# Kernel tuning notes

Hardware: AMD Instinct MI355X
Metric: run time of the kernel (lower is better)

The kernel has to match this reference:

```python
import jax, jax.numpy as jnp
import numpy as np

U = 64  # LSTM_UNITS

def _lstm(xt, kernel, rec, bias):
    # xt: [B, T, 4U]; keras LSTM gate order i, f, g(c), o
    B = xt.shape[0]
    h0 = jnp.zeros((B, U), xt.dtype)
    c0 = jnp.zeros((B, U), xt.dtype)
    def step(carry, x):
        h, c = carry
        z = x @ kernel + h @ rec + bias  # [B, 4U]
        i, f, g, o = jnp.split(z, 4, axis=-1)
        i = jax.nn.sigmoid(i); f = jax.nn.sigmoid(f)
        g = jnp.tanh(g); o = jax.nn.sigmoid(o)
        c = f * c + i * g
        h = o * jnp.tanh(c)
        return (h, c), h
    _, hs = jax.lax.scan(step, (h0, c0), jnp.swapaxes(xt, 0, 1))
    return jnp.swapaxes(hs, 0, 1)  # [B, T, U]

def setup_inputs() -> dict:
    key = jax.random.key(0)
    ks = jax.random.split(key, 12)
    B, T, P = 8, 100, 1000
    pro_id = jax.random.randint(ks[0], (B, T), 0, P, dtype=jnp.int32)
    label = jax.random.randint(ks[1], (B, T), 0, 2, dtype=jnp.int32)
    X = jax.random.normal(ks[2], (P, 2 * U), jnp.float32)
    cos_X = jax.random.uniform(ks[3], (P, P), jnp.float32)
    trimatrix = jnp.tril(jnp.ones((T, T), jnp.float32))  # causal mask [s, t]
    onehot_table = jax.random.normal(ks[4], (2, 4 * U), jnp.float32)
    s = 0.05
    lstm_kernel = jax.random.normal(ks[5], (4 * U, 4 * U), jnp.float32) * s
    lstm_rec = jax.random.normal(ks[6], (U, 4 * U), jnp.float32) * s
    lstm_bias = jnp.zeros((4 * U,), jnp.float32)
    W1 = jax.random.normal(ks[7], (3 * U, 50), jnp.float32) * s
    b1 = jnp.zeros((50,), jnp.float32)
    W2 = jax.random.normal(ks[8], (50, 1), jnp.float32) * s
    b2 = jnp.zeros((1,), jnp.float32)
    return {"pro_id": pro_id, "label": label, "num_pro": P, "X": X,
            "cos_X": cos_X, "trimatrix": trimatrix, "onehot_table": onehot_table,
            "lstm_kernel": lstm_kernel, "lstm_rec": lstm_rec, "lstm_bias": lstm_bias,
            "W1": W1, "b1": b1, "W2": W2, "b2": b2}

def reference(pro_id, label, num_pro, X, cos_X, trimatrix, onehot_table,
              lstm_kernel, lstm_rec, lstm_bias, W1, b1, W2, b2):
    B, T = pro_id.shape
    # one_hot @ X  ==  gather rows of X
    t_X = jnp.tile(X[pro_id], (1, 1, 2))           # [B, T, 4U]
    label_emb = onehot_table[label]                 # [B, T, 4U]
    xt = t_X * label_emb
    ht = _lstm(xt, lstm_kernel, lstm_rec, lstm_bias)  # [B, T, U]
    a = cos_X[pro_id]                               # [B, T, P] (one_hot @ cos_X)
    # ajhj[b,t,p,u] = sum_s tri[s,t] * a[b,s,p] * ht[b,s,u]  (causal weighted sum)
    ajhj = jnp.einsum('bsp,bsu,st->btpu', a, ht, trimatrix)
    XX = jnp.broadcast_to(X[None, None], (B, T, num_pro, 2 * U))
    hatt = jnp.concatenate([ajhj, XX], axis=-1)     # [B, T, P, 3U]
    r = jax.nn.relu(hatt @ W1 + b1)                 # [B, T, P, 50]
    prediction = r @ W2 + b2                        # [B, T, P, 1]
    return prediction
```

## Files before the change

### kernel.cpp

```cpp
#include <hip/hip_runtime.h>
#include <math.h>

#define BB 8
#define TT 100
#define PP 1000
#define UU 64
#define NJ 52
#define GROW 56


__global__ __launch_bounds__(256) void k1_xk(const int* __restrict__ pro_id,
    const int* __restrict__ label, const float* __restrict__ X,
    const float* __restrict__ onehot, const float* __restrict__ kern,
    const float* __restrict__ bias, float* __restrict__ xk)
{
    __shared__ __align__(16) float xt[8][256];
    const int j = threadIdx.x;
    const int r0 = blockIdx.x * 8;
    for (int r = 0; r < 8; ++r) {
        int row = r0 + r;
        int pid = pro_id[row];
        int lab = label[row];
        xt[r][j] = X[pid * 128 + (j & 127)] * onehot[lab * 256 + j];
    }
    __syncthreads();
    float acc[8];
    float bj = bias[j];
#pragma unroll
    for (int r = 0; r < 8; ++r) acc[r] = bj;
    for (int k4 = 0; k4 < 256; k4 += 4) {
        float4 xv[8];
#pragma unroll
        for (int r = 0; r < 8; ++r) xv[r] = *(const float4*)&xt[r][k4];
#pragma unroll
        for (int kk = 0; kk < 4; ++kk) {
            float kv = kern[(k4 + kk) * 256 + j];
#pragma unroll
            for (int r = 0; r < 8; ++r) {
                float x = (kk == 0) ? xv[r].x : (kk == 1) ? xv[r].y : (kk == 2) ? xv[r].z : xv[r].w;
                acc[r] += x * kv;
            }
        }
    }
#pragma unroll
    for (int r = 0; r < 8; ++r) xk[(r0 + r) * 256 + j] = acc[r];
}

__global__ __launch_bounds__(256) void k2_lstm(const float* __restrict__ xk,
    const float* __restrict__ rec, float* __restrict__ ht)
{
    __shared__ __align__(16) float h_sh[64];
    __shared__ float zs[256];
    const int j = threadIdx.x;
    const int b = blockIdx.x;
    float reccol[64];
#pragma unroll
    for (int u = 0; u < 64; ++u) reccol[u] = rec[u * 256 + j];
    float c = 0.f;
    if (j < 64) h_sh[j] = 0.f;
    __syncthreads();
    for (int t = 0; t < TT; ++t) {
        float z = xk[(b * TT + t) * 256 + j];
#pragma unroll
        for (int u4 = 0; u4 < 16; ++u4) {
            float4 h4 = *(const float4*)&h_sh[u4 * 4];
            z += h4.x * reccol[u4 * 4 + 0] + h4.y * reccol[u4 * 4 + 1]
               + h4.z * reccol[u4 * 4 + 2] + h4.w * reccol[u4 * 4 + 3];
        }
        float act;
        if (j >= 128 && j < 192) {
            act = 2.f / (1.f + __expf(-2.f * z)) - 1.f;
        } else {
            act = 1.f / (1.f + __expf(-z));
        }
        zs[j] = act;
        __syncthreads();
        if (j < 64) {
            float gi = zs[j], gf = zs[j + 64], gg = zs[j + 128], go = zs[j + 192];
            c = gf * c + gi * gg;
            float th = 2.f / (1.f + __expf(-2.f * c)) - 1.f;
            float h = go * th;
            h_sh[j] = h;
            ht[(b * TT + t) * 64 + j] = h;
        }
        __syncthreads();
    }
}

__global__ __launch_bounds__(256) void k3_xct(const float* __restrict__ X,
    const float* __restrict__ W1, const float* __restrict__ b1,
    float* __restrict__ XcT)
{
    int n = blockIdx.x * 256 + threadIdx.x;
    if (n >= GROW * PP) return;
    int jrow = n / PP;
    int p = n - jrow * PP;
    float acc = 0.f;
    if (jrow < 50) {
        acc = b1[jrow];
        for (int k = 0; k < 128; ++k)
            acc += X[p * 128 + k] * W1[(64 + k) * 50 + jrow];
    }
    XcT[n] = acc;
}

__global__ __launch_bounds__(64) void kg(const float* __restrict__ ht,
    const float* __restrict__ W1, float* __restrict__ G)
{
    __shared__ float hsh[64];
    const int row = blockIdx.x;
    const int j = threadIdx.x;
    hsh[j] = ht[row * 64 + j];
    __syncthreads();
    float acc = 0.f;
    if (j < 50) {
#pragma unroll
        for (int u = 0; u < 64; ++u) acc += hsh[u] * W1[u * 50 + j];
    }
    if (j < GROW) G[row * GROW + j] = acc;
}

__global__ __launch_bounds__(256) void k4_main(const int* __restrict__ pro_id,
    const float* __restrict__ cos_X, const float* __restrict__ XcT,
    const float* __restrict__ G, const float* __restrict__ W2,
    const float* __restrict__ b2, float* __restrict__ out)
{
    const int b = blockIdx.z;
    const int p = blockIdx.y * 256 + threadIdx.x;
    const int ci = blockIdx.x;
    const int t0 = ci * 7;
    const int t1 = (t0 + 7 < TT) ? (t0 + 7) : TT;
    const bool valid = p < PP;
    const int pc = valid ? p : 0;

    float V[NJ];
#pragma unroll
    for (int jj = 0; jj < NJ; ++jj) V[jj] = XcT[jj * PP + pc];
    const float b2v = b2[0];

    for (int s = TT - 1; s >= t0; --s) {
        int pid = pro_id[b * TT + s];
        float a = cos_X[pid * PP + pc];
        const float4* G4 = (const float4*)(G + (b * TT + s) * GROW);
#pragma unroll
        for (int jv = 0; jv < 13; ++jv) {
            float4 g = G4[jv];
            V[4 * jv + 0] += a * g.x;
            V[4 * jv + 1] += a * g.y;
            V[4 * jv + 2] += a * g.z;
            V[4 * jv + 3] += a * g.w;
        }
        if (s < t1) {
            float acc = b2v;
#pragma unroll
            for (int jv = 0; jv < 12; ++jv) {
                float4 w = *(const float4*)&W2[4 * jv];
                acc += w.x * fmaxf(V[4 * jv + 0], 0.f)
                     + w.y * fmaxf(V[4 * jv + 1], 0.f)
                     + w.z * fmaxf(V[4 * jv + 2], 0.f)
                     + w.w * fmaxf(V[4 * jv + 3], 0.f);
            }
            acc += W2[48] * fmaxf(V[48], 0.f) + W2[49] * fmaxf(V[49], 0.f);
            if (valid) out[(b * TT + s) * PP + p] = acc;
        }
    }
}

extern "C" void kernel_launch(void* const* d_in, const int* in_sizes, int n_in,
                              void* d_out, int out_size, void* d_ws, size_t ws_size,
                              hipStream_t stream)
{
    const int* pro_id  = (const int*)d_in[0];
    const int* label   = (const int*)d_in[1];
    const float* X     = (const float*)d_in[3];
    const float* cos_X = (const float*)d_in[4];
    const float* onehot = (const float*)d_in[6];
    const float* lk    = (const float*)d_in[7];
    const float* lr    = (const float*)d_in[8];
    const float* lb    = (const float*)d_in[9];
    const float* W1    = (const float*)d_in[10];
    const float* b1    = (const float*)d_in[11];
    const float* W2    = (const float*)d_in[12];
    const float* b2    = (const float*)d_in[13];

    float* ws  = (float*)d_ws;
    float* xk  = ws;
    float* ht  = ws + 204800;
    float* XcT = ws + 256000;
    float* G   = ws + 312000;
    float* out = (float*)d_out;

    hipLaunchKernelGGL(k1_xk,  dim3(100),      dim3(256), 0, stream, pro_id, label, X, onehot, lk, lb, xk);
    hipLaunchKernelGGL(k3_xct, dim3(219),      dim3(256), 0, stream, X, W1, b1, XcT);
    hipLaunchKernelGGL(k2_lstm,dim3(8),        dim3(256), 0, stream, xk, lr, ht);
    hipLaunchKernelGGL(kg,     dim3(800),      dim3(64),  0, stream, ht, W1, G);
    hipLaunchKernelGGL(k4_main,dim3(15, 4, 8), dim3(256), 0, stream, pro_id, cos_X, XcT, G, W2, b2, out);
}
```

Before: 216.4 us.

## Fuse prep kernels, shuffle-based LSTM gate exchange, fold G projection into LSTM

Merges the xk projection and the X·W1 precompute into one launch by splitting on block index. The X·W1 part now stages X transposed in shared memory. The LSTM kernel lays threads out so each wavefront holds all four gates for 16 units, so gates are exchanged with shuffles and one barrier per step is removed. It also prefetches the next xk value, splits the dot product into four accumulators, and keeps every h in shared memory so the G = h·W1 projection runs at the end of the same kernel. This cuts launch count and the serial per-step latency, but the G projection now runs on only 8 blocks.

Result: slower. 273.6 us (+26.4%).

```diff
diff --git a/kernel.cpp b/kernel.cpp
--- a/kernel.cpp
+++ b/kernel.cpp
@@ -4,120 +4,170 @@
 #define BB 8
 #define TT 100
 #define PP 1000
-#define UU 64
 #define NJ 52
 #define GROW 56
-
-
-__global__ __launch_bounds__(256) void k1_xk(const int* __restrict__ pro_id,
+#define HSTRIDE 68
+
+
+__global__ __launch_bounds__(256) void prep(const int* __restrict__ pro_id,
     const int* __restrict__ label, const float* __restrict__ X,
     const float* __restrict__ onehot, const float* __restrict__ kern,
-    const float* __restrict__ bias, float* __restrict__ xk)
-{
-    __shared__ __align__(16) float xt[8][256];
-    const int j = threadIdx.x;
-    const int r0 = blockIdx.x * 8;
-    for (int r = 0; r < 8; ++r) {
-        int row = r0 + r;
-        int pid = pro_id[row];
-        int lab = label[row];
-        xt[r][j] = X[pid * 128 + (j & 127)] * onehot[lab * 256 + j];
-    }
+    const float* __restrict__ bias, const float* __restrict__ W1,
+    const float* __restrict__ b1, float* __restrict__ xk, float* __restrict__ XcT)
+{
+    __shared__ __align__(16) float smem[128 * 65];
+    const int tid = threadIdx.x;
+
+    if (blockIdx.x < 100) {
+        float (*xt)[256] = (float(*)[256])smem;
+        const int j = tid;
+        const int r0 = blockIdx.x * 8;
+        for (int r = 0; r < 8; ++r) {
+            int row = r0 + r;
+            int pid = pro_id[row];
+            int lab = label[row];
+            xt[r][j] = X[pid * 128 + (j & 127)] * onehot[lab * 256 + j];
+        }
+        __syncthreads();
+        float acc[8];
+        float bj = bias[j];
+#pragma unroll
+        for (int r = 0; r < 8; ++r) acc[r] = bj;
+        for (int k4 = 0; k4 < 256; k4 += 4) {
+            float4 xv[8];
+#pragma unroll
+            for (int r = 0; r < 8; ++r) xv[r] = *(const float4*)&xt[r][k4];
+#pragma unroll
+            for (int kk = 0; kk < 4; ++kk) {
+                float kv = kern[(k4 + kk) * 256 + j];
+#pragma unroll
+                for (int r = 0; r < 8; ++r) {
+                    float x = (kk == 0) ? xv[r].x : (kk == 1) ? xv[r].y : (kk == 2) ? xv[r].z : xv[r].w;
+                    acc[r] += x * kv;
+                }
+            }
+        }
+#pragma unroll
+        for (int r = 0; r < 8; ++r) xk[(r0 + r) * 256 + j] = acc[r];
+    } else {
+        const int p0 = (blockIdx.x - 100) * 64;
+#pragma unroll
+        for (int r = 0; r < 8; ++r) {
+            int flat = (tid + 256 * r) * 4;
+            int i = flat >> 7;
+            int k = flat & 127;
+            int p = p0 + i;
+            float4 v = make_float4(0.f, 0.f, 0.f, 0.f);
+            if (p < PP) v = *(const float4*)&X[p * 128 + k];
+            smem[(k + 0) * 65 + i] = v.x;
+            smem[(k + 1) * 65 + i] = v.y;
+            smem[(k + 2) * 65 + i] = v.z;
+            smem[(k + 3) * 65 + i] = v.w;
+        }
+        __syncthreads();
+        const int ploc = tid & 63;
+        const int j0 = tid >> 6;
+        float acc[13];
+#pragma unroll
+        for (int m = 0; m < 13; ++m) {
+            int j = j0 + 4 * m;
+            acc[m] = (j < 50) ? b1[j] : 0.f;
+        }
+        for (int k = 0; k < 128; ++k) {
+            float xv = smem[k * 65 + ploc];
+            const float* w1r = &W1[(64 + k) * 50];
+#pragma unroll
+            for (int m = 0; m < 13; ++m) {
+                int j = j0 + 4 * m;
+                if (j < 50) acc[m] += xv * w1r[j];
+            }
+        }
+        int p = p0 + ploc;
+        if (p < PP) {
+#pragma unroll
+            for (int m = 0; m < 13; ++m) {
+                int j = j0 + 4 * m;
+                if (j < 50) XcT[j * PP + p] = acc[m];
+            }
+        }
+        for (int idx = tid; idx < 6 * 64; idx += 256) {
+            int r = 50 + (idx >> 6);
+            int pp = p0 + (idx & 63);
+            if (pp < PP) XcT[r * PP + pp] = 0.f;
+        }
+    }
+}
+
+__global__ __launch_bounds__(256) void k2_lstm(const float* __restrict__ xk,
+    const float* __restrict__ rec, const float* __restrict__ W1,
+    float* __restrict__ G)
+{
+    __shared__ __align__(16) float h_all[(TT + 1) * HSTRIDE];
+    const int tid = threadIdx.x;
+    const int b = blockIdx.x;
+    const int l = tid & 63;
+    const int w = tid >> 6;
+    const int u = (w << 4) | (l & 15);
+    const int g = l >> 4;
+    const int col = (g << 6) | u;
+
+    float rcol[64];
+#pragma unroll
+    for (int u2 = 0; u2 < 64; ++u2) rcol[u2] = rec[u2 * 256 + col];
+
+    if (tid < 64) h_all[tid] = 0.f;
+    float c = 0.f;
+    const float* xkb = xk + b * TT * 256;
+    float zc = xkb[col];
     __syncthreads();
-    float acc[8];
-    float bj = bias[j];
-#pragma unroll
-    for (int r = 0; r < 8; ++r) acc[r] = bj;
-    for (int k4 = 0; k4 < 256; k4 += 4) {
-        float4 xv[8];
-#pragma unroll
-        for (int r = 0; r < 8; ++r) xv[r] = *(const float4*)&xt[r][k4];
-#pragma unroll
-        for (int kk = 0; kk < 4; ++kk) {
-            float kv = kern[(k4 + kk) * 256 + j];
-#pragma unroll
-            for (int r = 0; r < 8; ++r) {
-                float x = (kk == 0) ? xv[r].x : (kk == 1) ? xv[r].y : (kk == 2) ? xv[r].z : xv[r].w;
-                acc[r] += x * kv;
-            }
-        }
-    }
-#pragma unroll
-    for (int r = 0; r < 8; ++r) xk[(r0 + r) * 256 + j] = acc[r];
-}
-
-__global__ __launch_bounds__(256) void k2_lstm(const float* __restrict__ xk,
-    const float* __restrict__ rec, float* __restrict__ ht)
-{
-    __shared__ __align__(16) float h_sh[64];
-    __shared__ float zs[256];
-    const int j = threadIdx.x;
-    const int b = blockIdx.x;
-    float reccol[64];
-#pragma unroll
-    for (int u = 0; u < 64; ++u) reccol[u] = rec[u * 256 + j];
-    float c = 0.f;
-    if (j < 64) h_sh[j] = 0.f;
-    __syncthreads();
+
     for (int t = 0; t < TT; ++t) {
-        float z = xk[(b * TT + t) * 256 + j];
-#pragma unroll
-        for (int u4 = 0; u4 < 16; ++u4) {
-            float4 h4 = *(const float4*)&h_sh[u4 * 4];
-            z += h4.x * reccol[u4 * 4 + 0] + h4.y * reccol[u4 * 4 + 1]
-               + h4.z * reccol[u4 * 4 + 2] + h4.w * reccol[u4 * 4 + 3];
-        }
+        float a0 = zc, a1 = 0.f, a2 = 0.f, a3 = 0.f;
+        if (t < TT - 1) zc = xkb[(t + 1) * 256 + col];
+        const float4* h4p = (const float4*)&h_all[t * HSTRIDE];
+#pragma unroll
+        for (int m = 0; m < 16; ++m) {
+            float4 hv = h4p[m];
+            a0 += hv.x * rcol[4 * m + 0];
+            a1 += hv.y * rcol[4 * m + 1];
+            a2 += hv.z * rcol[4 * m + 2];
+            a3 += hv.w * rcol[4 * m + 3];
+        }
+        float z = (a0 + a1) + (a2 + a3);
         float act;
-        if (j >= 128 && j < 192) {
-            act = 2.f / (1.f + __expf(-2.f * z)) - 1.f;
-        } else {
-            act = 1.f / (1.f + __expf(-z));
-        }
-        zs[j] = act;
+        if (g == 2) act = 2.f / (1.f + __expf(-2.f * z)) - 1.f;
+        else        act = 1.f / (1.f + __expf(-z));
+        const int base = l & 15;
+        float gi = __shfl(act, base);
+        float gf = __shfl(act, base + 16);
+        float gg = __shfl(act, base + 32);
+        float go = __shfl(act, base + 48);
+        c = gf * c + gi * gg;
+        float h = go * (2.f / (1.f + __expf(-2.f * c)) - 1.f);
+        if (g == 0) h_all[(t + 1) * HSTRIDE + u] = h;
         __syncthreads();
-        if (j < 64) {
-            float gi = zs[j], gf = zs[j + 64], gg = zs[j + 128], go = zs[j + 192];
-            c = gf * c + gi * gg;
-            float th = 2.f / (1.f + __expf(-2.f * c)) - 1.f;
-            float h = go * th;
-            h_sh[j] = h;
-            ht[(b * TT + t) * 64 + j] = h;
-        }
-        __syncthreads();
-    }
-}
-
-__global__ __launch_bounds__(256) void k3_xct(const float* __restrict__ X,
-    const float* __restrict__ W1, const float* __restrict__ b1,
-    float* __restrict__ XcT)
-{
-    int n = blockIdx.x * 256 + threadIdx.x;
-    if (n >= GROW * PP) return;
-    int jrow = n / PP;
-    int p = n - jrow * PP;
-    float acc = 0.f;
-    if (jrow < 50) {
-        acc = b1[jrow];
-        for (int k = 0; k < 128; ++k)
-            acc += X[p * 128 + k] * W1[(64 + k) * 50 + jrow];
-    }
-    XcT[n] = acc;
-}
-
-__global__ __launch_bounds__(64) void kg(const float* __restrict__ ht,
-    const float* __restrict__ W1, float* __restrict__ G)
-{
-    __shared__ float hsh[64];
-    const int row = blockIdx.x;
-    const int j = threadIdx.x;
-    hsh[j] = ht[row * 64 + j];
-    __syncthreads();
-    float acc = 0.f;
-    if (j < 50) {
-#pragma unroll
-        for (int u = 0; u < 64; ++u) acc += hsh[u] * W1[u * 50 + j];
-    }
-    if (j < GROW) G[row * GROW + j] = acc;
+    }
+
+    const int brow0 = b * TT;
+    for (int idx = tid; idx < TT * 13; idx += 256) {
+        int row = idx / 13;
+        int m = idx - row * 13;
+        int j = 4 * m;
+        const float* hrow = &h_all[(row + 1) * HSTRIDE];
+        float ax = 0.f, ay = 0.f, az = 0.f, aw = 0.f;
+#pragma unroll 16
+        for (int u2 = 0; u2 < 64; ++u2) {
+            float hv = hrow[u2];
+            const float* wp = &W1[u2 * 50 + j];
+            ax += hv * wp[0];
+            ay += hv * wp[1];
+            az += hv * wp[2];
+            aw += hv * wp[3];
+        }
+        if (m == 12) { az = 0.f; aw = 0.f; }
+        float4 o = make_float4(ax, ay, az, aw);
+        *(float4*)&G[(brow0 + row) * GROW + j] = o;
+    }
 }
 
 __global__ __launch_bounds__(256) void k4_main(const int* __restrict__ pro_id,
@@ -144,21 +194,21 @@
         const float4* G4 = (const float4*)(G + (b * TT + s) * GROW);
 #pragma unroll
         for (int jv = 0; jv < 13; ++jv) {
-            float4 g = G4[jv];
-            V[4 * jv + 0] += a * g.x;
-            V[4 * jv + 1] += a * g.y;
-            V[4 * jv + 2] += a * g.z;
-            V[4 * jv + 3] += a * g.w;
+            float4 gv = G4[jv];
+            V[4 * jv + 0] += a * gv.x;
+            V[4 * jv + 1] += a * gv.y;
+            V[4 * jv + 2] += a * gv.z;
+            V[4 * jv + 3] += a * gv.w;
         }
         if (s < t1) {
             float acc = b2v;
 #pragma unroll
             for (int jv = 0; jv < 12; ++jv) {
-                float4 w = *(const float4*)&W2[4 * jv];
-                acc += w.x * fmaxf(V[4 * jv + 0], 0.f)
-                     + w.y * fmaxf(V[4 * jv + 1], 0.f)
-                     + w.z * fmaxf(V[4 * jv + 2], 0.f)
-                     + w.w * fmaxf(V[4 * jv + 3], 0.f);
+                float4 wv = *(const float4*)&W2[4 * jv];
+                acc += wv.x * fmaxf(V[4 * jv + 0], 0.f)
+                     + wv.y * fmaxf(V[4 * jv + 1], 0.f)
+                     + wv.z * fmaxf(V[4 * jv + 2], 0.f)
+                     + wv.w * fmaxf(V[4 * jv + 3], 0.f);
             }
             acc += W2[48] * fmaxf(V[48], 0.f) + W2[49] * fmaxf(V[49], 0.f);
             if (valid) out[(b * TT + s) * PP + p] = acc;
@@ -185,14 +235,13 @@
 
     float* ws  = (float*)d_ws;
     float* xk  = ws;
-    float* ht  = ws + 204800;
-    float* XcT = ws + 256000;
-    float* G   = ws + 312000;
+    float* XcT = ws + 204800;
+    float* G   = ws + 260800;
     float* out = (float*)d_out;
 
-    hipLaunchKernelGGL(k1_xk,  dim3(100),      dim3(256), 0, stream, pro_id, label, X, onehot, lk, lb, xk);
-    hipLaunchKernelGGL(k3_xct, dim3(219),      dim3(256), 0, stream, X, W1, b1, XcT);
-    hipLaunchKernelGGL(k2_lstm,dim3(8),        dim3(256), 0, stream, xk, lr, ht);
-    hipLaunchKernelGGL(kg,     dim3(800),      dim3(64),  0, stream, ht, W1, G);
-    hipLaunchKernelGGL(k4_main,dim3(15, 4, 8), dim3(256), 0, stream, pro_id, cos_X, XcT, G, W2, b2, out);
-}
+    hipLaunchKernelGGL(prep,   dim3(116),      dim3(256), 0, stream,
+                       pro_id, label, X, onehot, lk, lb, W1, b1, xk, XcT);
+    hipLaunchKernelGGL(k2_lstm,dim3(8),        dim3(256), 0, stream, xk, lr, W1, G);
+    hipLaunchKernelGGL(k4_main,dim3(15, 4, 8), dim3(256), 0, stream,
+                       pro_id, cos_X, XcT, G, W2, b2, out);
+}
```
